# Kernel optimization log

Measured on AMD Instinct MI355X. Metric: run time of the kernel, lower is better.

Reference implementation:

```python
import jax, jax.numpy as jnp
import numpy as np

N_EMBD = 1024
N_HEAD = 16
B, T = 4, 2048


def setup_inputs() -> dict:
    key = jax.random.key(0)
    ks = jax.random.split(key, 4)
    s = 1.0 / np.sqrt(N_EMBD)
    return {
        "x": jax.random.normal(ks[0], (B, T, N_EMBD), dtype=jnp.float32),
        "w_attn": jax.random.normal(ks[1], (N_EMBD, 3 * N_EMBD), dtype=jnp.float32) * s,
        "b_attn": jnp.zeros((3 * N_EMBD,), dtype=jnp.float32),
        "w_proj": jax.random.normal(ks[2], (N_EMBD, N_EMBD), dtype=jnp.float32) * s,
        "b_proj": jnp.zeros((N_EMBD,), dtype=jnp.float32),
    }


def reference(x, w_attn, b_attn, w_proj, b_proj):
    Bb, Tt, C = x.shape
    H = N_HEAD
    D = C // H  # head dim
    qkv = x @ w_attn + b_attn  # [B,T,3C]
    q, k, v = jnp.split(qkv, 3, axis=2)
    # [B,H,T,D]
    q = q.reshape(Bb, Tt, H, D).transpose(0, 2, 1, 3)
    k = k.reshape(Bb, Tt, H, D).transpose(0, 2, 1, 3)
    v = v.reshape(Bb, Tt, H, D).transpose(0, 2, 1, 3)
    scale = 1.0 / np.sqrt(D).astype(np.float32)
    attn = jnp.einsum("bhqd,bhkd->bhqk", q, k) * scale
    mask = jnp.tril(jnp.ones((Tt, Tt), dtype=bool))
    attn = jnp.where(mask, attn, jnp.float32(-jnp.inf))
    probs = jax.nn.softmax(attn, axis=-1)
    out = jnp.einsum("bhqk,bhkd->bhqd", probs, v)
    out = out.transpose(0, 2, 1, 3).reshape(Bb, Tt, C)
    return out @ w_proj + b_proj
```

## Files before the change

### kernel.cpp

```cpp
#include <hip/hip_runtime.h>
#include <hip/hip_bf16.h>


typedef float f32x4 __attribute__((ext_vector_type(4)));
typedef float f32x16 __attribute__((ext_vector_type(16)));
typedef short short8 __attribute__((ext_vector_type(8)));
typedef short short4v __attribute__((ext_vector_type(4)));

__device__ __forceinline__ short f2bf(float f) {
  union { __hip_bfloat16 h; short s; } u;
  u.h = __float2bfloat16(f);
  return u.s;
}

__device__ __forceinline__ void gl_lds16(const void* g, void* l) {
  __builtin_amdgcn_global_load_lds(
      (const __attribute__((address_space(1))) void*)g,
      (__attribute__((address_space(3))) void*)l, 16, 0, 0);
}

__global__ void prep(const float* __restrict__ x, const float* __restrict__ wa,
                     const float* __restrict__ wp, short* __restrict__ xb,
                     short* __restrict__ wat, short* __restrict__ wpt) {
  const int bid = blockIdx.x, tid = threadIdx.x;
  if (bid < 8192) {
    int i = (bid * 256 + tid) * 4;
    float4 v = *(const float4*)(x + i);
    short4v o;
    o[0] = f2bf(v.x); o[1] = f2bf(v.y); o[2] = f2bf(v.z); o[3] = f2bf(v.w);
    *(short4v*)(xb + i) = o;
    return;
  }
  __shared__ float tile[32][33];
  const float* in;
  short* out;
  int N, bx, by;
  if (bid < 11264) {
    int t = bid - 8192;
    in = wa; out = wat; N = 3072; bx = t % 96; by = t / 96;
  } else {
    int t = bid - 11264;
    in = wp; out = wpt; N = 1024; bx = t & 31; by = t >> 5;
  }
  int tx = tid & 31, ty = tid >> 5;
  int x0 = bx * 32, y0 = by * 32;
#pragma unroll
  for (int i = 0; i < 32; i += 8)
    tile[ty + i][tx] = in[(size_t)(y0 + ty + i) * N + x0 + tx];
  __syncthreads();
#pragma unroll
  for (int i = 0; i < 32; i += 8)
    out[(size_t)(x0 + ty + i) * 1024 + y0 + tx] = f2bf(tile[tx][ty + i]);
}


#define GEMM_BODY(A_, Bt_)                                                        \
  __shared__ __align__(16) short As[128 * 32];                                    \
  __shared__ __align__(16) short Bs[128 * 32];                                    \
  const int tid = threadIdx.x;                                                    \
  const int wv = tid >> 6;                                                        \
  const int wr = wv >> 1, wc = wv & 1;                                            \
  const int col = tid & 31, khalf = (tid >> 5) & 1;                               \
  const int m0 = blockIdx.y * 128, n0 = blockIdx.x * 128;                         \
  f32x16 acc[2][2];                                                               \
  _Pragma("unroll") for (int i = 0; i < 2; ++i)                                   \
      _Pragma("unroll") for (int j = 0; j < 2; ++j)                               \
          acc[i][j] = (f32x16)(0.f);                                              \
  for (int k0 = 0; k0 < 1024; k0 += 32) {                                         \
    _Pragma("unroll") for (int i = 0; i < 2; ++i) {                               \
      int cc = tid + i * 256;                                                     \
      int row = cc >> 2, part = ((cc & 3) - ((cc >> 3) & 3)) & 3;                 \
      gl_lds16(A_ + (size_t)(m0 + row) * 1024 + k0 + part * 8,                    \
               (char*)As + cc * 16);                                              \
      gl_lds16(Bt_ + (size_t)(n0 + row) * 1024 + k0 + part * 8,                   \
               (char*)Bs + cc * 16);                                              \
    }                                                                             \
    __syncthreads();                                                              \
    short8 af[2][2], bf[2][2];                                                    \
    _Pragma("unroll") for (int i = 0; i < 2; ++i)                                 \
        _Pragma("unroll") for (int s = 0; s < 2; ++s) {                           \
          int pa = s * 2 + khalf;                                                 \
          int ra = wr * 64 + i * 32 + col;                                        \
          int rb = wc * 64 + i * 32 + col;                                        \
          af[i][s] = *(const short8*)&As[(ra * 4 + ((pa + (ra >> 1)) & 3)) * 8];  \
          bf[i][s] = *(const short8*)&Bs[(rb * 4 + ((pa + (rb >> 1)) & 3)) * 8];  \
        }                                                                         \
    _Pragma("unroll") for (int s = 0; s < 2; ++s)                                 \
        _Pragma("unroll") for (int i = 0; i < 2; ++i)                             \
            _Pragma("unroll") for (int j = 0; j < 2; ++j)                         \
                acc[i][j] = __builtin_amdgcn_mfma_f32_32x32x16_bf16(              \
                    af[i][s], bf[j][s], acc[i][j], 0, 0, 0);                      \
    __syncthreads();                                                              \
  }

__global__ __launch_bounds__(256, 2) void gemm_qkv(
    const short* __restrict__ A, const short* __restrict__ Bt,
    const float* __restrict__ bias, short* __restrict__ Qb,
    short* __restrict__ Kb, short* __restrict__ Vtb) {
  GEMM_BODY(A, Bt)
  const int rhalf = khalf * 4;
#pragma unroll
  for (int i = 0; i < 2; ++i) {
#pragma unroll
    for (int j = 0; j < 2; ++j) {
      int n = n0 + wc * 64 + j * 32 + col;
      int n2 = n & 1023;
      int hh = n2 >> 6, d = n2 & 63;
      float bv = bias[n];
      int mb = m0 + wr * 64 + i * 32 + rhalf;
      int bb = mb >> 11;
      int bh = (bb << 4) + hh;
      if (n < 2048) {
        const bool isq = n < 1024;
#pragma unroll
        for (int a = 0; a < 16; ++a) {
          int t = (mb + (a & 3) + 8 * (a >> 2)) & 2047;
          float o = acc[i][j][a] + bv;
          size_t idx = ((size_t)bh * 2048 + t) * 64 + d;
          if (isq)
            Qb[idx] = f2bf(o * 0.18033688f);
          else
            Kb[idx] = f2bf(o);
        }
      } else {
#pragma unroll
        for (int g = 0; g < 4; ++g) {
          int t = (mb + 8 * g) & 2047;
          short4v o;
#pragma unroll
          for (int r = 0; r < 4; ++r) o[r] = f2bf(acc[i][j][g * 4 + r] + bv);
          *(short4v*)&Vtb[((size_t)bh * 64 + d) * 2048 + t] = o;
        }
      }
    }
  }
}

__global__ __launch_bounds__(256, 2) void gemm_proj(
    const short* __restrict__ A, const short* __restrict__ Bt,
    const float* __restrict__ bias, float* __restrict__ out) {
  GEMM_BODY(A, Bt)
  const int rhalf = khalf * 4;
#pragma unroll
  for (int i = 0; i < 2; ++i) {
#pragma unroll
    for (int j = 0; j < 2; ++j) {
      int n = n0 + wc * 64 + j * 32 + col;
      float bv = bias[n];
      int mb = m0 + wr * 64 + i * 32 + rhalf;
#pragma unroll
      for (int a = 0; a < 16; ++a) {
        int m = mb + (a & 3) + 8 * (a >> 2);
        out[(size_t)m * 1024 + n] = acc[i][j][a] + bv;
      }
    }
  }
}

__global__ __launch_bounds__(256, 2) void flash_attn(
    const short* __restrict__ Qg_, const short* __restrict__ Kg_,
    const short* __restrict__ Vg_, short* __restrict__ Ob) {
  constexpr int STR = 72;
  __shared__ __align__(16) short Kl[2][64 * STR];
  __shared__ __align__(16) short Vl[2][64 * STR];
  const int tid = threadIdx.x;
  const int wv = tid >> 6, ln = tid & 15, quad = (tid & 63) >> 4;
  const int bh = blockIdx.x & 63;
  const int pair = blockIdx.x >> 6;
  const short* Qg = Qg_ + (size_t)bh * 2048 * 64;
  const short* Kg = Kg_ + (size_t)bh * 2048 * 64;
  const short* Vg = Vg_ + (size_t)bh * 64 * 2048;
  const int srow = tid >> 3, spart = tid & 7;
  const int bb = bh >> 4, hh = bh & 15;

  short8 kreg[2], vreg[2];

#define LOADKV(KT)                                                              \
  {                                                                             \
    const short* Kt = Kg + (size_t)(KT) * 64 * 64;                              \
    _Pragma("unroll") for (int i = 0; i < 2; ++i) {                             \
      kreg[i] = *(const short8*)(Kt + (size_t)(srow + i * 32) * 64 + spart * 8);\
      vreg[i] = *(const short8*)(Vg + (size_t)(srow + i * 32) * 2048 +          \
                                 (KT) * 64 + spart * 8);                        \
    }                                                                           \
  }
#define WRITEKV(BUF)                                                            \
  _Pragma("unroll") for (int i = 0; i < 2; ++i) {                               \
    *(short8*)&Kl[BUF][(srow + i * 32) * STR + spart * 8] = kreg[i];            \
    *(short8*)&Vl[BUF][(srow + i * 32) * STR + spart * 8] = vreg[i];            \
  }

#pragma unroll
  for (int it = 0; it < 2; ++it) {
    const int qt = it ? pair : (15 - pair);
    const int q0 = qt * 128;
    const int qbase = q0 + wv * 32;
    const int nkt = (q0 >> 6) + 2;

    short8 qf[2][2];
#pragma unroll
    for (int h = 0; h < 2; ++h)
#pragma unroll
      for (int ch = 0; ch < 2; ++ch)
        qf[h][ch] = *(const short8*)(Qg + (size_t)(qbase + h * 16 + ln) * 64 +
                                     ch * 32 + quad * 8);

    f32x4 Oacc[2][4];
#pragma unroll
    for (int h = 0; h < 2; ++h)
#pragma unroll
      for (int mt = 0; mt < 4; ++mt) Oacc[h][mt] = (f32x4){0.f, 0.f, 0.f, 0.f};
    float lpart[2] = {0.f, 0.f};

    LOADKV(0)
    __syncthreads();
    WRITEKV(0)
    LOADKV(1)

    for (int kt = 0; kt < nkt; ++kt) {
      __syncthreads();
      const short* Kcur = Kl[kt & 1];
      const short* Vcur = Vl[kt & 1];
      if (kt + 1 < nkt) {
        WRITEKV((kt + 1) & 1)
        if (kt + 2 < nkt) LOADKV(kt + 2)
      }

      if (kt * 64 <= qbase + 31) {
        f32x4 St[2][4];
#pragma unroll
        for (int h = 0; h < 2; ++h)
#pragma unroll
          for (int kb = 0; kb < 4; ++kb) St[h][kb] = (f32x4){0.f, 0.f, 0.f, 0.f};
#pragma unroll
        for (int kb = 0; kb < 4; ++kb) {
          short8 ka0 = *(const short8*)&Kcur[(kb * 16 + ln) * STR + quad * 8];
          short8 ka1 = *(const short8*)&Kcur[(kb * 16 + ln) * STR + 32 + quad * 8];
#pragma unroll
          for (int h = 0; h < 2; ++h) {
            St[h][kb] = __builtin_amdgcn_mfma_f32_16x16x32_bf16(
                ka0, qf[h][0], St[h][kb], 0, 0, 0);
            St[h][kb] = __builtin_amdgcn_mfma_f32_16x16x32_bf16(
                ka1, qf[h][1], St[h][kb], 0, 0, 0);
          }
        }

        short4v pf[2][4];
#pragma unroll
        for (int h = 0; h < 2; ++h) {
          float lp0 = 0.f, lp1 = 0.f;
          if (kt * 64 + 63 <= qbase + h * 16) {
#pragma unroll
            for (int kb = 0; kb < 4; ++kb) {
              float p[4];
#pragma unroll
              for (int r = 0; r < 4; ++r)
                p[r] = __builtin_amdgcn_exp2f(St[h][kb][r]);
              lp0 += p[0] + p[2];
              lp1 += p[1] + p[3];
              union { __hip_bfloat162 b2; unsigned u; } w0, w1;
              w0.b2 = __float22bfloat162_rn(make_float2(p[0], p[1]));
              w1.b2 = __float22bfloat162_rn(make_float2(p[2], p[3]));
              union { short4v s4; unsigned u2[2]; } m;
              m.u2[0] = w0.u; m.u2[1] = w1.u;
              pf[h][kb] = m.s4;
            }
          } else {
            const int qg = qbase + h * 16 + ln;
#pragma unroll
            for (int kb = 0; kb < 4; ++kb) {
              float p[4];
#pragma unroll
              for (int r = 0; r < 4; ++r) {
                int key = kt * 64 + kb * 16 + quad * 4 + r;
                float s = (key <= qg) ? St[h][kb][r] : -1e30f;
                p[r] = __builtin_amdgcn_exp2f(s);
              }
              lp0 += p[0] + p[2];
              lp1 += p[1] + p[3];
              union { __hip_bfloat162 b2; unsigned u; } w0, w1;
              w0.b2 = __float22bfloat162_rn(make_float2(p[0], p[1]));
              w1.b2 = __float22bfloat162_rn(make_float2(p[2], p[3]));
              union { short4v s4; unsigned u2[2]; } m;
              m.u2[0] = w0.u; m.u2[1] = w1.u;
              pf[h][kb] = m.s4;
            }
          }
          lpart[h] += lp0 + lp1;
        }

#pragma unroll
        for (int kb = 0; kb < 4; ++kb)
#pragma unroll
          for (int mt = 0; mt < 4; ++mt) {
            short4v va =
                *(const short4v*)&Vcur[(mt * 16 + ln) * STR + kb * 16 + quad * 4];
#pragma unroll
            for (int h = 0; h < 2; ++h)
              Oacc[h][mt] = __builtin_amdgcn_mfma_f32_16x16x16bf16_1k(
                  va, pf[h][kb], Oacc[h][mt], 0, 0, 0);
          }
      }
    }

#pragma unroll
    for (int h = 0; h < 2; ++h) {
      float l = lpart[h];
      l += __shfl_xor(l, 16);
      l += __shfl_xor(l, 32);
      float rl = 1.0f / l;
      int t = qbase + h * 16 + ln;
#pragma unroll
      for (int mt = 0; mt < 4; ++mt) {
        short4v o;
#pragma unroll
        for (int r = 0; r < 4; ++r) o[r] = f2bf(Oacc[h][mt][r] * rl);
        *(short4v*)(Ob + ((size_t)(bb * 2048 + t)) * 1024 + hh * 64 + mt * 16 +
                    quad * 4) = o;
      }
    }
  }
#undef LOADKV
#undef WRITEKV
}


extern "C" void kernel_launch(void* const* d_in, const int* in_sizes, int n_in,
                              void* d_out, int out_size, void* d_ws, size_t ws_size,
                              hipStream_t stream) {
  const float* x      = (const float*)d_in[0];
  const float* w_attn = (const float*)d_in[1];
  const float* b_attn = (const float*)d_in[2];
  const float* w_proj = (const float*)d_in[3];
  const float* b_proj = (const float*)d_in[4];
  float* out = (float*)d_out;
  char* ws = (char*)d_ws;

  short* xb  = (short*)(ws);
  short* wat = (short*)(ws + 16777216);
  short* wpt = (short*)(ws + 23068672);
  short* Qb  = (short*)(ws + 25165824);
  short* Kb  = (short*)(ws + 41943040);
  short* Vtb = (short*)(ws + 58720256);
  short* Ob  = (short*)(ws + 75497472);

  prep<<<12288, 256, 0, stream>>>(x, w_attn, w_proj, xb, wat, wpt);
  gemm_qkv<<<dim3(24, 64), 256, 0, stream>>>(xb, wat, b_attn, Qb, Kb, Vtb);
  flash_attn<<<512, 256, 0, stream>>>(Qb, Kb, Vtb, Ob);
  gemm_proj<<<dim3(8, 64), 256, 0, stream>>>(Ob, wpt, b_proj, out);
}
```

Before: 257.2 us.

## Rewrite QKV GEMM with 256x256 tiles, 8 waves, and double-buffered async LDS pipeline

The QKV projection GEMM moves from 128x128 tiles with 4 waves and single-buffered LDS to 256x256 tiles with 8 waves. It stages K-chunks of 64 into double-buffered LDS through direct global-to-LDS loads, using manual vmcnt/lgkmcnt waits and barriers so the next tile loads while MFMAs run. It also switches to 16x16x32 MFMAs and raises wave priority around MFMA bursts. The aim is more data reuse per tile and hiding memory latency, at the cost of large LDS use (128KB per block) and fewer blocks (384) for the CUs.

```diff
diff --git a/kernel.cpp b/kernel.cpp
--- a/kernel.cpp
+++ b/kernel.cpp
@@ -52,7 +52,6 @@
   for (int i = 0; i < 32; i += 8)
     out[(size_t)(x0 + ty + i) * 1024 + y0 + tx] = f2bf(tile[tx][ty + i]);
 }
-
 
 #define GEMM_BODY(A_, Bt_)                                                        \
   __shared__ __align__(16) short As[128 * 32];                                    \
@@ -93,29 +92,144 @@
     __syncthreads();                                                              \
   }
 
-__global__ __launch_bounds__(256, 2) void gemm_qkv(
+__global__ __launch_bounds__(256, 2) void gemm_proj(
+    const short* __restrict__ A, const short* __restrict__ Bt,
+    const float* __restrict__ bias, float* __restrict__ out) {
+  GEMM_BODY(A, Bt)
+  const int rhalf = khalf * 4;
+#pragma unroll
+  for (int i = 0; i < 2; ++i) {
+#pragma unroll
+    for (int j = 0; j < 2; ++j) {
+      int n = n0 + wc * 64 + j * 32 + col;
+      float bv = bias[n];
+      int mb = m0 + wr * 64 + i * 32 + rhalf;
+#pragma unroll
+      for (int a = 0; a < 16; ++a) {
+        int m = mb + (a & 3) + 8 * (a >> 2);
+        out[(size_t)m * 1024 + n] = acc[i][j][a] + bv;
+      }
+    }
+  }
+}
+
+
+#define LGKM0() asm volatile("s_waitcnt lgkmcnt(0)" ::: "memory")
+#define BARRIER() asm volatile("s_barrier" ::: "memory")
+
+#define STG(KT, S, SRC, LB)                                                \
+  if ((KT) < 16) {                                                         \
+    char* db_ = (char*)(LB) + (((KT) & 1) ? 32768 : 0) + ((S) * 16384);    \
+    const short* sb_ = (SRC) + (KT) * 64 + (S) * 32;                       \
+    gl_lds16(sb_ + g_off0, db_ + d_off0);                                  \
+    gl_lds16(sb_ + g_off1, db_ + d_off1);                                  \
+  }
+
+#define LDA(S, MH)                                                         \
+  _Pragma("unroll") for (int mt_ = 0; mt_ < 4; ++mt_)                      \
+      af[mt_] = *(const short8*)(Ab + (S)*16384 + (MH)*4096 + arow_off +   \
+                                 mt_ * 1024);
+
+#define LDB(S)                                                             \
+  _Pragma("unroll") for (int nt_ = 0; nt_ < 4; ++nt_)                      \
+      bf[nt_] = *(const short8*)(Bb + (S)*16384 + brow_off + nt_ * 1024);
+
+#define MFMA16(MH)                                                         \
+  LGKM0();                                                                 \
+  __builtin_amdgcn_s_setprio(1);                                           \
+  _Pragma("unroll") for (int mt_ = 0; mt_ < 4; ++mt_)                      \
+      _Pragma("unroll") for (int nt_ = 0; nt_ < 4; ++nt_)                  \
+          acc[(MH)*4 + mt_][nt_] =                                         \
+              __builtin_amdgcn_mfma_f32_16x16x32_bf16(                     \
+                  af[mt_], bf[nt_], acc[(MH)*4 + mt_][nt_], 0, 0, 0);      \
+  __builtin_amdgcn_s_setprio(0);
+
+__global__ __launch_bounds__(512, 2) void gemm_qkv(
     const short* __restrict__ A, const short* __restrict__ Bt,
     const float* __restrict__ bias, short* __restrict__ Qb,
     short* __restrict__ Kb, short* __restrict__ Vtb) {
-  GEMM_BODY(A, Bt)
-  const int rhalf = khalf * 4;
-#pragma unroll
-  for (int i = 0; i < 2; ++i) {
-#pragma unroll
-    for (int j = 0; j < 2; ++j) {
-      int n = n0 + wc * 64 + j * 32 + col;
-      int n2 = n & 1023;
-      int hh = n2 >> 6, d = n2 & 63;
-      float bv = bias[n];
-      int mb = m0 + wr * 64 + i * 32 + rhalf;
-      int bb = mb >> 11;
-      int bh = (bb << 4) + hh;
+  __shared__ __align__(16) short Asm[2][16384];
+  __shared__ __align__(16) short Bsm[2][16384];
+  const int tid = threadIdx.x;
+  const int wv = tid >> 6;
+  const int wr = wv >> 2, wc = wv & 3;
+  const int ln16 = tid & 15, q4 = (tid >> 4) & 3;
+  const int m0 = blockIdx.y * 256, n0 = blockIdx.x * 256;
+
+  const int d_off0 = tid * 16, d_off1 = d_off0 + 8192;
+  const size_t g_off0 = (size_t)(tid >> 2) * 1024 + (size_t)(tid & 3) * 8;
+  const size_t g_off1 = g_off0 + (size_t)128 * 1024;
+
+  const int arow_off = (wr * 128 + ln16) * 64 + q4 * 16;
+  const int brow_off = (wc * 64 + ln16) * 64 + q4 * 16;
+
+  const short* srcA = A + (size_t)m0 * 1024;
+  const short* srcB = Bt + (size_t)n0 * 1024;
+
+  f32x4 acc[8][4];
+#pragma unroll
+  for (int i = 0; i < 8; ++i)
+#pragma unroll
+    for (int j = 0; j < 4; ++j) acc[i][j] = (f32x4){0.f, 0.f, 0.f, 0.f};
+
+  STG(0, 0, srcA, Asm)
+  STG(0, 0, srcB, Bsm)
+  STG(0, 1, srcA, Asm)
+  STG(0, 1, srcB, Bsm)
+  STG(1, 0, srcA, Asm)
+  STG(1, 0, srcB, Bsm)
+  asm volatile("s_waitcnt vmcnt(4)" ::: "memory");
+  BARRIER();
+
+  for (int kt = 0; kt < 16; ++kt) {
+    const char* Ab = (const char*)Asm + ((kt & 1) ? 32768 : 0);
+    const char* Bb = (const char*)Bsm + ((kt & 1) ? 32768 : 0);
+    short8 af[4], bf[4];
+    LDB(0)
+    LDA(0, 0)
+    STG(kt + 1, 1, srcA, Asm)
+    BARRIER();
+    MFMA16(0)
+    BARRIER();
+    LDA(0, 1)
+    STG(kt + 1, 1, srcB, Bsm)
+    BARRIER();
+    MFMA16(1)
+    BARRIER();
+    LDB(1)
+    LDA(1, 0)
+    STG(kt + 2, 0, srcA, Asm)
+    BARRIER();
+    MFMA16(0)
+    BARRIER();
+    LDA(1, 1)
+    STG(kt + 2, 0, srcB, Bsm)
+    BARRIER();
+    MFMA16(1)
+    if (kt == 14) {
+      asm volatile("s_waitcnt vmcnt(0)" ::: "memory");
+    } else {
+      asm volatile("s_waitcnt vmcnt(4)" ::: "memory");
+    }
+    BARRIER();
+  }
+
+#pragma unroll
+  for (int nt = 0; nt < 4; ++nt) {
+    int n = n0 + wc * 64 + nt * 16 + ln16;
+    float bv = bias[n];
+    int n2 = n & 1023;
+    int hcol = n2 >> 6, d = n2 & 63;
+#pragma unroll
+    for (int i = 0; i < 8; ++i) {
+      int mb = m0 + wr * 128 + (i >> 2) * 64 + (i & 3) * 16 + q4 * 4;
+      int bh = ((mb >> 11) << 4) + hcol;
       if (n < 2048) {
         const bool isq = n < 1024;
 #pragma unroll
-        for (int a = 0; a < 16; ++a) {
-          int t = (mb + (a & 3) + 8 * (a >> 2)) & 2047;
-          float o = acc[i][j][a] + bv;
+        for (int r = 0; r < 4; ++r) {
+          int t = (mb + r) & 2047;
+          float o = acc[i][nt][r] + bv;
           size_t idx = ((size_t)bh * 2048 + t) * 64 + d;
           if (isq)
             Qb[idx] = f2bf(o * 0.18033688f);
@@ -123,35 +237,11 @@
             Kb[idx] = f2bf(o);
         }
       } else {
-#pragma unroll
-        for (int g = 0; g < 4; ++g) {
-          int t = (mb + 8 * g) & 2047;
-          short4v o;
-#pragma unroll
-          for (int r = 0; r < 4; ++r) o[r] = f2bf(acc[i][j][g * 4 + r] + bv);
-          *(short4v*)&Vtb[((size_t)bh * 64 + d) * 2048 + t] = o;
-        }
-      }
-    }
-  }
-}
-
-__global__ __launch_bounds__(256, 2) void gemm_proj(
-    const short* __restrict__ A, const short* __restrict__ Bt,
-    const float* __restrict__ bias, float* __restrict__ out) {
-  GEMM_BODY(A, Bt)
-  const int rhalf = khalf * 4;
-#pragma unroll
-  for (int i = 0; i < 2; ++i) {
-#pragma unroll
-    for (int j = 0; j < 2; ++j) {
-      int n = n0 + wc * 64 + j * 32 + col;
-      float bv = bias[n];
-      int mb = m0 + wr * 64 + i * 32 + rhalf;
-#pragma unroll
-      for (int a = 0; a < 16; ++a) {
-        int m = mb + (a & 3) + 8 * (a >> 2);
-        out[(size_t)m * 1024 + n] = acc[i][j][a] + bv;
+        int t = mb & 2047;
+        short4v o;
+#pragma unroll
+        for (int r = 0; r < 4; ++r) o[r] = f2bf(acc[i][nt][r] + bv);
+        *(short4v*)&Vtb[((size_t)bh * 64 + d) * 2048 + t] = o;
       }
     }
   }
@@ -345,7 +435,7 @@
   short* Ob  = (short*)(ws + 75497472);
 
   prep<<<12288, 256, 0, stream>>>(x, w_attn, w_proj, xb, wat, wpt);
-  gemm_qkv<<<dim3(24, 64), 256, 0, stream>>>(xb, wat, b_attn, Qb, Kb, Vtb);
+  gemm_qkv<<<dim3(12, 32), 512, 0, stream>>>(xb, wat, b_attn, Qb, Kb, Vtb);
   flash_attn<<<512, 256, 0, stream>>>(Qb, Kb, Vtb, Ob);
   gemm_proj<<<dim3(8, 64), 256, 0, stream>>>(Ob, wpt, b_proj, out);
 }
```

Result: slower. 264.8 us (+3.0%).

## Rewrite QKV GEMM with 256x256 tiles, 8 waves and double-buffered LDS pipeline

Applied to the files above, without the earlier changes.

The QKV projection GEMM moves from 128x128 tiles with 4 waves to 256x256 tiles with 8 waves, with K-chunks of 64 double-buffered in LDS. Global-to-LDS loads for later stages are interleaved with MFMA blocks, using explicit vmcnt/lgkmcnt waits, raw s_barrier and setprio. The goal is to overlap memory and compute and to raise data reuse per tile. In exchange the kernel uses 128KB of LDS and launches only 384 blocks, which limits occupancy and may leave CUs unevenly loaded.

```diff
diff --git a/kernel.cpp b/kernel.cpp
--- a/kernel.cpp
+++ b/kernel.cpp
@@ -52,7 +52,6 @@
   for (int i = 0; i < 32; i += 8)
     out[(size_t)(x0 + ty + i) * 1024 + y0 + tx] = f2bf(tile[tx][ty + i]);
 }
-
 
 #define GEMM_BODY(A_, Bt_)                                                        \
   __shared__ __align__(16) short As[128 * 32];                                    \
@@ -93,21 +92,163 @@
     __syncthreads();                                                              \
   }
 
-__global__ __launch_bounds__(256, 2) void gemm_qkv(
+__global__ __launch_bounds__(256, 2) void gemm_proj(
+    const short* __restrict__ A, const short* __restrict__ Bt,
+    const float* __restrict__ bias, float* __restrict__ out) {
+  GEMM_BODY(A, Bt)
+  const int rhalf = khalf * 4;
+#pragma unroll
+  for (int i = 0; i < 2; ++i) {
+#pragma unroll
+    for (int j = 0; j < 2; ++j) {
+      int n = n0 + wc * 64 + j * 32 + col;
+      float bv = bias[n];
+      int mb = m0 + wr * 64 + i * 32 + rhalf;
+#pragma unroll
+      for (int a = 0; a < 16; ++a) {
+        int m = mb + (a & 3) + 8 * (a >> 2);
+        out[(size_t)m * 1024 + n] = acc[i][j][a] + bv;
+      }
+    }
+  }
+}
+
+
+#define BARRIER() asm volatile("s_barrier" ::: "memory")
+#define VMC(N) asm volatile("s_waitcnt vmcnt(" #N ")" ::: "memory")
+
+#define STG(KT, S, SRC, LB)                                                \
+  if ((KT) < 16) {                                                         \
+    char* db_ = (char*)(LB) + (((KT) & 1) ? 32768 : 0) + ((S) * 16384);    \
+    const short* sb_ = (SRC) + (KT) * 64 + (S) * 32;                       \
+    gl_lds16(sb_ + g_off0, db_ + d_off0);                                  \
+    gl_lds16(sb_ + g_off1, db_ + d_off1);                                  \
+  }
+
+#define LDF(AF, BF, ABP, BBP, S, AO, BO)                                   \
+  _Pragma("unroll") for (int mt_ = 0; mt_ < 4; ++mt_)                      \
+      AF[mt_] = *(const short8*)((ABP) + (S) * 16384 + (AO)[mt_]);         \
+  _Pragma("unroll") for (int nt_ = 0; nt_ < 2; ++nt_)                      \
+      BF[nt_] = *(const short8*)((BBP) + (S) * 16384 + (BO)[nt_]);
+
+#define MFMA8_BODY(AF, BF)                                                 \
+  __builtin_amdgcn_sched_barrier(0);                                       \
+  __builtin_amdgcn_s_setprio(1);                                           \
+  _Pragma("unroll") for (int mt_ = 0; mt_ < 4; ++mt_)                      \
+      _Pragma("unroll") for (int nt_ = 0; nt_ < 2; ++nt_)                  \
+          acc[mt_][nt_] = __builtin_amdgcn_mfma_f32_32x32x16_bf16(         \
+              AF[mt_], BF[nt_], acc[mt_][nt_], 0, 0, 0);                   \
+  __builtin_amdgcn_s_setprio(0);
+
+#define MFMA8(AF, BF)                                                      \
+  __builtin_amdgcn_sched_barrier(0);                                       \
+  asm volatile("s_waitcnt lgkmcnt(6)" ::: "memory");                       \
+  MFMA8_BODY(AF, BF)
+
+#define MFMA8_LG0(AF, BF)                                                  \
+  __builtin_amdgcn_sched_barrier(0);                                       \
+  asm volatile("s_waitcnt lgkmcnt(0)" ::: "memory");                       \
+  MFMA8_BODY(AF, BF)
+
+__global__ __launch_bounds__(512, 2) void gemm_qkv(
     const short* __restrict__ A, const short* __restrict__ Bt,
     const float* __restrict__ bias, short* __restrict__ Qb,
     short* __restrict__ Kb, short* __restrict__ Vtb) {
-  GEMM_BODY(A, Bt)
+  __shared__ __align__(16) short Asm[2][16384];
+  __shared__ __align__(16) short Bsm[2][16384];
+  const int tid = threadIdx.x;
+  const int wv = tid >> 6;
+  const int wr = wv >> 2, wc = wv & 3;
+  const int ln32 = tid & 31, khalf = (tid >> 5) & 1;
+  const int m0 = blockIdx.y * 256, n0 = blockIdx.x * 256;
+
+  const int d_off0 = tid * 16, d_off1 = d_off0 + 8192;
+  const int pa_st = ((tid & 3) - ((tid >> 3) & 3)) & 3;
+  const size_t g_off0 = (size_t)(tid >> 2) * 1024 + (size_t)pa_st * 8;
+  const size_t g_off1 = g_off0 + (size_t)128 * 1024;
+
+  const int rot = (ln32 >> 1) & 3;
+  const int slotE = (khalf + rot) & 3;
+  const int slotO = (2 + khalf + rot) & 3;
+  int aoffE[4], aoffO[4], boffE[2], boffO[2];
+#pragma unroll
+  for (int mt = 0; mt < 4; ++mt) {
+    int r = (wr * 128 + mt * 32 + ln32) * 64;
+    aoffE[mt] = r + slotE * 16;
+    aoffO[mt] = r + slotO * 16;
+  }
+#pragma unroll
+  for (int nt = 0; nt < 2; ++nt) {
+    int r = (wc * 64 + nt * 32 + ln32) * 64;
+    boffE[nt] = r + slotE * 16;
+    boffO[nt] = r + slotO * 16;
+  }
+
+  const short* srcA = A + (size_t)m0 * 1024;
+  const short* srcB = Bt + (size_t)n0 * 1024;
+
+  f32x16 acc[4][2];
+#pragma unroll
+  for (int i = 0; i < 4; ++i)
+#pragma unroll
+    for (int j = 0; j < 2; ++j) acc[i][j] = (f32x16)(0.f);
+
+  short8 af0[4], af1[4], bf0[2], bf1[2];
+
+  STG(0, 0, srcA, Asm)
+  STG(0, 0, srcB, Bsm)
+  STG(0, 1, srcA, Asm)
+  STG(0, 1, srcB, Bsm)
+  STG(1, 0, srcA, Asm)
+  STG(1, 0, srcB, Bsm)
+  VMC(8);
+  BARRIER();
+  {
+    const char* Ab0 = (const char*)Asm;
+    const char* Bb0 = (const char*)Bsm;
+    LDF(af0, bf0, Ab0, Bb0, 0, aoffE, boffE)
+  }
+
+  for (int kt = 0; kt < 16; ++kt) {
+    const char* Ab = (const char*)Asm + ((kt & 1) << 15);
+    const char* Bb = (const char*)Bsm + ((kt & 1) << 15);
+    const char* An = (const char*)Asm + (((kt + 1) & 1) << 15);
+    const char* Bn = (const char*)Bsm + (((kt + 1) & 1) << 15);
+    LDF(af1, bf1, Ab, Bb, 0, aoffO, boffO)
+    STG(kt + 1, 1, srcA, Asm)
+    MFMA8(af0, bf0)
+    if (kt == 15) { VMC(0); } else { VMC(6); }
+    BARRIER();
+    LDF(af0, bf0, Ab, Bb, 1, aoffE, boffE)
+    STG(kt + 1, 1, srcB, Bsm)
+    MFMA8(af1, bf1)
+    BARRIER();
+    LDF(af1, bf1, Ab, Bb, 1, aoffO, boffO)
+    STG(kt + 2, 0, srcA, Asm)
+    MFMA8(af0, bf0)
+    if (kt == 14) { VMC(4); } else if (kt < 14) { VMC(6); }
+    BARRIER();
+    if (kt < 15) {
+      LDF(af0, bf0, An, Bn, 0, aoffE, boffE)
+      STG(kt + 2, 0, srcB, Bsm)
+      MFMA8(af1, bf1)
+    } else {
+      MFMA8_LG0(af1, bf1)
+    }
+    BARRIER();
+  }
+
+  const int col = tid & 31;
   const int rhalf = khalf * 4;
 #pragma unroll
-  for (int i = 0; i < 2; ++i) {
+  for (int i = 0; i < 4; ++i) {
 #pragma unroll
     for (int j = 0; j < 2; ++j) {
       int n = n0 + wc * 64 + j * 32 + col;
       int n2 = n & 1023;
       int hh = n2 >> 6, d = n2 & 63;
       float bv = bias[n];
-      int mb = m0 + wr * 64 + i * 32 + rhalf;
+      int mb = m0 + wr * 128 + i * 32 + rhalf;
       int bb = mb >> 11;
       int bh = (bb << 4) + hh;
       if (n < 2048) {
@@ -131,27 +272,6 @@
           for (int r = 0; r < 4; ++r) o[r] = f2bf(acc[i][j][g * 4 + r] + bv);
           *(short4v*)&Vtb[((size_t)bh * 64 + d) * 2048 + t] = o;
         }
-      }
-    }
-  }
-}
-
-__global__ __launch_bounds__(256, 2) void gemm_proj(
-    const short* __restrict__ A, const short* __restrict__ Bt,
-    const float* __restrict__ bias, float* __restrict__ out) {
-  GEMM_BODY(A, Bt)
-  const int rhalf = khalf * 4;
-#pragma unroll
-  for (int i = 0; i < 2; ++i) {
-#pragma unroll
-    for (int j = 0; j < 2; ++j) {
-      int n = n0 + wc * 64 + j * 32 + col;
-      float bv = bias[n];
-      int mb = m0 + wr * 64 + i * 32 + rhalf;
-#pragma unroll
-      for (int a = 0; a < 16; ++a) {
-        int m = mb + (a & 3) + 8 * (a >> 2);
-        out[(size_t)m * 1024 + n] = acc[i][j][a] + bv;
       }
     }
   }
@@ -345,7 +465,7 @@
   short* Ob  = (short*)(ws + 75497472);
 
   prep<<<12288, 256, 0, stream>>>(x, w_attn, w_proj, xb, wat, wpt);
-  gemm_qkv<<<dim3(24, 64), 256, 0, stream>>>(xb, wat, b_attn, Qb, Kb, Vtb);
+  gemm_qkv<<<dim3(12, 32), 512, 0, stream>>>(xb, wat, b_attn, Qb, Kb, Vtb);
   flash_attn<<<512, 256, 0, stream>>>(Qb, Kb, Vtb, Ob);
   gemm_proj<<<dim3(8, 64), 256, 0, stream>>>(Ob, wpt, b_proj, out);
 }
```

Result: no change. 255.3 us (-0.7%).

## Double-buffer GEMM LDS tiles and raise wave priority around attention MFMAs

Applied to the files above, without the earlier changes.

The shared GEMM body now keeps two LDS buffers for the A and B tiles. It issues the global-to-LDS loads for the next k-step before running the MFMAs on the current one, and precomputes the global offsets once. The aim is to hide global memory latency behind matrix math instead of stalling at a barrier every k-step. The change doubles the LDS used per block. Separately, the attention kernel raises wave priority with s_setprio around its QK^T and PV MFMA blocks, so that matrix work gets issue preference over the softmax sections of other waves.

```diff
diff --git a/kernel.cpp b/kernel.cpp
--- a/kernel.cpp
+++ b/kernel.cpp
@@ -55,35 +55,49 @@
 
 
 #define GEMM_BODY(A_, Bt_)                                                        \
-  __shared__ __align__(16) short As[128 * 32];                                    \
-  __shared__ __align__(16) short Bs[128 * 32];                                    \
+  __shared__ __align__(16) short As[2][128 * 32];                                 \
+  __shared__ __align__(16) short Bs[2][128 * 32];                                 \
   const int tid = threadIdx.x;                                                    \
   const int wv = tid >> 6;                                                        \
   const int wr = wv >> 1, wc = wv & 1;                                            \
   const int col = tid & 31, khalf = (tid >> 5) & 1;                               \
   const int m0 = blockIdx.y * 128, n0 = blockIdx.x * 128;                         \
+  const int cc0 = tid, cc1 = tid + 256;                                           \
+  const int row0 = cc0 >> 2, part0 = ((cc0 & 3) - ((cc0 >> 3) & 3)) & 3;          \
+  const int row1 = cc1 >> 2, part1 = ((cc1 & 3) - ((cc1 >> 3) & 3)) & 3;          \
+  const size_t ga0 = (size_t)(m0 + row0) * 1024 + part0 * 8;                      \
+  const size_t ga1 = (size_t)(m0 + row1) * 1024 + part1 * 8;                      \
+  const size_t gb0 = (size_t)(n0 + row0) * 1024 + part0 * 8;                      \
+  const size_t gb1 = (size_t)(n0 + row1) * 1024 + part1 * 8;                      \
   f32x16 acc[2][2];                                                               \
   _Pragma("unroll") for (int i = 0; i < 2; ++i)                                   \
       _Pragma("unroll") for (int j = 0; j < 2; ++j)                               \
           acc[i][j] = (f32x16)(0.f);                                              \
-  for (int k0 = 0; k0 < 1024; k0 += 32) {                                         \
-    _Pragma("unroll") for (int i = 0; i < 2; ++i) {                               \
-      int cc = tid + i * 256;                                                     \
-      int row = cc >> 2, part = ((cc & 3) - ((cc >> 3) & 3)) & 3;                 \
-      gl_lds16(A_ + (size_t)(m0 + row) * 1024 + k0 + part * 8,                    \
-               (char*)As + cc * 16);                                              \
-      gl_lds16(Bt_ + (size_t)(n0 + row) * 1024 + k0 + part * 8,                   \
-               (char*)Bs + cc * 16);                                              \
+  gl_lds16(A_ + ga0, (char*)As[0] + cc0 * 16);                                    \
+  gl_lds16(A_ + ga1, (char*)As[0] + cc1 * 16);                                    \
+  gl_lds16(Bt_ + gb0, (char*)Bs[0] + cc0 * 16);                                   \
+  gl_lds16(Bt_ + gb1, (char*)Bs[0] + cc1 * 16);                                   \
+  __syncthreads();                                                                \
+  for (int kt = 0; kt < 32; ++kt) {                                               \
+    if (kt + 1 < 32) {                                                            \
+      const int k0 = (kt + 1) * 32;                                               \
+      char* Ad = (char*)As[(kt + 1) & 1];                                         \
+      char* Bd = (char*)Bs[(kt + 1) & 1];                                         \
+      gl_lds16(A_ + ga0 + k0, Ad + cc0 * 16);                                     \
+      gl_lds16(A_ + ga1 + k0, Ad + cc1 * 16);                                     \
+      gl_lds16(Bt_ + gb0 + k0, Bd + cc0 * 16);                                    \
+      gl_lds16(Bt_ + gb1 + k0, Bd + cc1 * 16);                                    \
     }                                                                             \
-    __syncthreads();                                                              \
+    const short* Ac = As[kt & 1];                                                 \
+    const short* Bc = Bs[kt & 1];                                                 \
     short8 af[2][2], bf[2][2];                                                    \
     _Pragma("unroll") for (int i = 0; i < 2; ++i)                                 \
         _Pragma("unroll") for (int s = 0; s < 2; ++s) {                           \
           int pa = s * 2 + khalf;                                                 \
           int ra = wr * 64 + i * 32 + col;                                        \
           int rb = wc * 64 + i * 32 + col;                                        \
-          af[i][s] = *(const short8*)&As[(ra * 4 + ((pa + (ra >> 1)) & 3)) * 8];  \
-          bf[i][s] = *(const short8*)&Bs[(rb * 4 + ((pa + (rb >> 1)) & 3)) * 8];  \
+          af[i][s] = *(const short8*)&Ac[(ra * 4 + ((pa + (ra >> 1)) & 3)) * 8];  \
+          bf[i][s] = *(const short8*)&Bc[(rb * 4 + ((pa + (rb >> 1)) & 3)) * 8];  \
         }                                                                         \
     _Pragma("unroll") for (int s = 0; s < 2; ++s)                                 \
         _Pragma("unroll") for (int i = 0; i < 2; ++i)                             \
@@ -232,6 +246,7 @@
         for (int h = 0; h < 2; ++h)
 #pragma unroll
           for (int kb = 0; kb < 4; ++kb) St[h][kb] = (f32x4){0.f, 0.f, 0.f, 0.f};
+        __builtin_amdgcn_s_setprio(1);
 #pragma unroll
         for (int kb = 0; kb < 4; ++kb) {
           short8 ka0 = *(const short8*)&Kcur[(kb * 16 + ln) * STR + quad * 8];
@@ -244,6 +259,7 @@
                 ka1, qf[h][1], St[h][kb], 0, 0, 0);
           }
         }
+        __builtin_amdgcn_s_setprio(0);
 
         short4v pf[2][4];
 #pragma unroll
@@ -289,6 +305,7 @@
           lpart[h] += lp0 + lp1;
         }
 
+        __builtin_amdgcn_s_setprio(1);
 #pragma unroll
         for (int kb = 0; kb < 4; ++kb)
 #pragma unroll
@@ -300,6 +317,7 @@
               Oacc[h][mt] = __builtin_amdgcn_mfma_f32_16x16x16bf16_1k(
                   va, pf[h][kb], Oacc[h][mt], 0, 0, 0);
           }
+        __builtin_amdgcn_s_setprio(0);
       }
     }
 
```

Result: no change. 255.9 us (-0.5%).
